# Kernel optimization log

Measured on AMD Instinct MI355X. Metric: run time of the kernel, lower is better.

The kernel has to match this reference:

```python
import jax, jax.numpy as jnp
import numpy as np

CAPACITY = 0.5  # top_k = int(seq_len * capacity)

def setup_inputs() -> dict:
    key = jax.random.key(0)
    k1, k2, k3, k4 = jax.random.split(key, 4)
    b, s, d, d_ff = 4, 4096, 1024, 4096
    x = jax.random.normal(k1, (b, s, d), dtype=jnp.float32)
    mask = jnp.ones((b, s), dtype=jnp.bool_)
    # learned params: router (Linear(d,1,bias=False)) and the block MLP
    Wr = jax.random.normal(k2, (d, 1), dtype=jnp.float32) * (d ** -0.5)
    W1 = jax.random.normal(k3, (d, d_ff), dtype=jnp.float32) * (d ** -0.5)
    W2 = jax.random.normal(k4, (d_ff, d), dtype=jnp.float32) * (d_ff ** -0.5)
    return {"x": x, "mask": mask, "Wr": Wr, "W1": W1, "W2": W2}

def reference(x, mask, Wr, W1, W2):
    b, s, d = x.shape
    top_k = int(s * CAPACITY)
    # router logits [b, s]
    logits = (x @ Wr)[..., 0]
    # top-k over sequence dim (torch sorted=False; softmax/gather are
    # permutation-equivariant so sorted top_k gives identical results)
    vals, idx = jax.lax.top_k(logits, top_k)          # [b, k]
    order = jnp.argsort(idx, axis=1)                  # sort selected indices ascending
    sel = jnp.take_along_axis(idx, order, axis=1)     # [b, k] token positions, ascending
    w = jax.nn.softmax(vals, axis=1)                  # softmax over selected logits
    r_w = jnp.take_along_axis(w, order, axis=1)       # weights reordered to match sel
    # gather selected tokens
    fx = jnp.take_along_axis(x, sel[..., None], axis=1)  # [b, k, d]
    # block: residual MLP whose update is scaled by router weights (mask unused by MLP)
    h = jax.nn.silu(fx @ W1) @ W2
    out = fx + h * r_w[..., None]
    # scatter processed tokens back into x
    batch = jnp.arange(b)[:, None]
    hidden_states = x.at[batch, sel].set(out)
    # aux loss: faithful to the original (flat view + flat index set, then BCE-with-logits mean)
    flat_logits = logits.reshape(-1)                  # [b*s]
    targets = jnp.zeros_like(flat_logits).at[sel.reshape(-1)].set(1.0)
    aux_loss = jnp.mean(
        jnp.maximum(flat_logits, 0.0)
        - flat_logits * targets
        + jnp.log1p(jnp.exp(-jnp.abs(flat_logits)))
    )
    return hidden_states, aux_loss
```

## Files before the change

kernel.cpp:

```cpp
#include <hip/hip_runtime.h>
#include <hip/hip_bf16.h>
#include <cstdint>

#define B_ 4
#define S_ 4096
#define D_ 1024
#define DFF_ 4096
#define KSEL_ 2048
#define M_ (B_ * KSEL_)
#define NTOK_ (B_ * S_)

typedef short bf16x8 __attribute__((ext_vector_type(8)));
typedef float f32x4 __attribute__((ext_vector_type(4)));

__device__ inline unsigned short f2bf(float f) {
    union { float f; unsigned int u; } c; c.f = f;
    unsigned int u = c.u;
    unsigned int r = u + 0x7fffu + ((u >> 16) & 1u);
    return (unsigned short)(r >> 16);
}

__global__ __launch_bounds__(256)
void transpose_bf16(const float* __restrict__ src, unsigned short* __restrict__ dst,
                    int R, int C) {
    __shared__ float tile[32][33];
    int c0 = blockIdx.x * 32, r0 = blockIdx.y * 32;
    for (int i = threadIdx.y; i < 32; i += 8)
        tile[i][threadIdx.x] = src[(size_t)(r0 + i) * C + c0 + threadIdx.x];
    __syncthreads();
    for (int i = threadIdx.y; i < 32; i += 8)
        dst[(size_t)(c0 + i) * R + r0 + threadIdx.x] = f2bf(tile[threadIdx.x][i]);
}

__global__ __launch_bounds__(256)
void router_kernel(const float* __restrict__ x, const float* __restrict__ Wr,
                   float* __restrict__ logits, unsigned short* __restrict__ xb,
                   float* __restrict__ out) {
    int wid = threadIdx.x >> 6, lane = threadIdx.x & 63;
    int row = blockIdx.x * 4 + wid;
    const float* xr = x + (size_t)row * D_;
    unsigned short* xbr = xb + (size_t)row * D_;
    float* outr = out + (size_t)row * D_;
    float acc = 0.f;
#pragma unroll
    for (int j = 0; j < 4; j++) {
        int off = j * 256 + lane * 4;
        float4 v = *(const float4*)(xr + off);
        float4 w = *(const float4*)(Wr + off);
        acc += v.x * w.x + v.y * w.y + v.z * w.z + v.w * w.w;
        *(float4*)(outr + off) = v;
        ushort4 o;
        o.x = f2bf(v.x); o.y = f2bf(v.y); o.z = f2bf(v.z); o.w = f2bf(v.w);
        *(ushort4*)(xbr + off) = o;
    }
#pragma unroll
    for (int s = 32; s; s >>= 1) acc += __shfl_xor(acc, s);
    if (lane == 0) logits[row] = acc;
}

__global__ __launch_bounds__(256)
void rank_partial_kernel(const float* __restrict__ logits, int* __restrict__ rank) {
    __shared__ float lj[512];
    int b  = blockIdx.x >> 7;
    int ic = (blockIdx.x >> 3) & 15;
    int jc = blockIdx.x & 7;
    const float* L = logits + b * S_;
    for (int t = threadIdx.x; t < 512; t += 256) lj[t] = L[jc * 512 + t];
    __syncthreads();
    int i = ic * 256 + threadIdx.x;
    float li = L[i];
    int jbase = jc * 512;
    int r = 0;
    const float4* __restrict__ lj4 = (const float4*)lj;
#pragma unroll 4
    for (int q = 0; q < 128; q++) {
        float4 v = lj4[q];
        int jb = jbase + q * 4;
        r += (v.x > li) | ((v.x == li) & (jb     < i));
        r += (v.y > li) | ((v.y == li) & (jb + 1 < i));
        r += (v.z > li) | ((v.z == li) & (jb + 2 < i));
        r += (v.w > li) | ((v.w == li) & (jb + 3 < i));
    }
    atomicAdd(&rank[b * S_ + i], r);
}

__global__ __launch_bounds__(256)
void compact_kernel(const float* __restrict__ logits, const int* __restrict__ rank,
                    int* __restrict__ flags,
                    int* __restrict__ rowidx, float* __restrict__ rw) {
    __shared__ float lg[S_];
    __shared__ int f[S_];
    __shared__ int tsum[256];
    __shared__ float red[256];
    int b = blockIdx.x;
    const float* L = logits + b * S_;
    const int* R = rank + b * S_;
    int* F = flags + b * S_;
    for (int j = threadIdx.x; j < S_ / 4; j += 256) {
        ((float4*)lg)[j] = ((const float4*)L)[j];
        int4 rk = ((const int4*)R)[j];
        int4 fl;
        fl.x = rk.x < KSEL_; fl.y = rk.y < KSEL_;
        fl.z = rk.z < KSEL_; fl.w = rk.w < KSEL_;
        ((int4*)f)[j] = fl;
        ((int4*)F)[j] = fl;
    }
    __syncthreads();
    float mx = -INFINITY;
    for (int j = threadIdx.x; j < S_; j += 256) mx = fmaxf(mx, lg[j]);
    red[threadIdx.x] = mx; __syncthreads();
    for (int s = 128; s; s >>= 1) {
        if (threadIdx.x < s) red[threadIdx.x] = fmaxf(red[threadIdx.x], red[threadIdx.x + s]);
        __syncthreads();
    }
    float m = red[0];
    __syncthreads();

    float esum = 0.f;
    int s0 = 0;
#pragma unroll
    for (int j = 0; j < 16; j++) {
        int i = threadIdx.x * 16 + j;
        s0 += f[i];
        if (f[i]) esum += expf(lg[i] - m);
    }
    red[threadIdx.x] = esum; __syncthreads();
    for (int s = 128; s; s >>= 1) {
        if (threadIdx.x < s) red[threadIdx.x] += red[threadIdx.x + s];
        __syncthreads();
    }
    float inv = 1.f / red[0];

    tsum[threadIdx.x] = s0; __syncthreads();
    for (int s = 1; s < 256; s <<= 1) {
        int u = (threadIdx.x >= s) ? tsum[threadIdx.x - s] : 0;
        __syncthreads();
        tsum[threadIdx.x] += u;
        __syncthreads();
    }
    int pos = tsum[threadIdx.x] - s0;
    for (int j = 0; j < 16; j++) {
        int i = threadIdx.x * 16 + j;
        if (f[i]) {
            rowidx[b * KSEL_ + pos] = b * S_ + i;
            rw[b * KSEL_ + pos] = expf(lg[i] - m) * inv;
            pos++;
        }
    }
}

__global__ __launch_bounds__(256)
void loss_kernel(const float* __restrict__ logits, const int* __restrict__ flags,
                 float* __restrict__ partials) {
    __shared__ float red[256];
    int i = blockIdx.x * 256 + threadIdx.x;
    float l = logits[i];
    float t = 0.f;
    if (i < S_)
        t = (flags[i] | flags[S_ + i] | flags[2 * S_ + i] | flags[3 * S_ + i]) ? 1.f : 0.f;
    float v = fmaxf(l, 0.f) - l * t + log1pf(expf(-fabsf(l)));
    red[threadIdx.x] = v; __syncthreads();
    for (int s = 128; s; s >>= 1) {
        if (threadIdx.x < s) red[threadIdx.x] += red[threadIdx.x + s];
        __syncthreads();
    }
    if (threadIdx.x == 0) partials[blockIdx.x] = red[0];
}

__global__ void loss_final(const float* __restrict__ partials, float* __restrict__ out) {
    float v = partials[threadIdx.x];
#pragma unroll
    for (int s = 32; s; s >>= 1) v += __shfl_xor(v, s);
    if (threadIdx.x == 0) out[0] = v / (float)NTOK_;
}

template <int MODE>
__global__ __launch_bounds__(256)
void gemm_bt_kernel(const unsigned short* __restrict__ A,
                    const unsigned short* __restrict__ BT,
                    const int* __restrict__ rowidx,
                    const float* __restrict__ rw,
                    const float* __restrict__ x,
                    unsigned short* __restrict__ Hout,
                    float* __restrict__ Out,
                    int K, int N) {
    __shared__ __attribute__((aligned(16))) unsigned short As[128 * 64];
    __shared__ __attribute__((aligned(16))) unsigned short Bs[128 * 64];
    const int tid = threadIdx.x;
    const int w = tid >> 6, lane = tid & 63;
    const int wm = w >> 1, wn = w & 1;
    const int tile_m = blockIdx.y * 128;
    const int tile_n = blockIdx.x * 128;

    const int srow = lane >> 3;
    const int sw = (lane & 7) ^ srow;
    const uint64_t abase = (uint64_t)(uintptr_t)A;
    const uint64_t bbase = (uint64_t)(uintptr_t)BT;
    uint64_t aaddr[4], baddr[4];
#pragma unroll
    for (int t = 0; t < 4; ++t) {
        int r = t * 32 + w * 8 + srow;
        int am = tile_m + r;
        int ar = (MODE == 1) ? rowidx[am] : am;
        aaddr[t] = abase + ((uint64_t)ar * K + (uint64_t)sw * 8) * 2ull;
        int bn = tile_n + r;
        baddr[t] = bbase + ((uint64_t)bn * K + (uint64_t)sw * 8) * 2ull;
    }

    f32x4 acc[4][4];
#pragma unroll
    for (int i = 0; i < 4; i++)
#pragma unroll
        for (int j = 0; j < 4; j++) acc[i][j] = (f32x4){0.f, 0.f, 0.f, 0.f};

    const int lr = lane & 15, quad = lane >> 4;
    const int KI = K >> 6;
    for (int it = 0; it < KI; ++it) {
        const uint64_t koff = (uint64_t)(it * 64) * 2ull;
#pragma unroll
        for (int t = 0; t < 4; ++t) {
            unsigned short* ldsA = &As[(t * 32 + w * 8) * 64];
            unsigned short* ldsB = &Bs[(t * 32 + w * 8) * 64];
            __builtin_amdgcn_global_load_lds(
                (const __attribute__((address_space(1))) unsigned int*)(uintptr_t)(aaddr[t] + koff),
                (__attribute__((address_space(3))) unsigned int*)ldsA, 16, 0, 0);
            __builtin_amdgcn_global_load_lds(
                (const __attribute__((address_space(1))) unsigned int*)(uintptr_t)(baddr[t] + koff),
                (__attribute__((address_space(3))) unsigned int*)ldsB, 16, 0, 0);
        }
        __syncthreads();
#pragma unroll
        for (int ks = 0; ks < 2; ++ks) {
            bf16x8 af[4], bfr[4];
#pragma unroll
            for (int t4 = 0; t4 < 4; ++t4) {
                int row = wm * 64 + t4 * 16 + lr;
                int kc = ks * 4 + quad;
                af[t4] = *(const bf16x8*)((const char*)As + row * 128 + ((kc ^ (lr & 7)) * 16));
                int nr = wn * 64 + t4 * 16 + lr;
                bfr[t4] = *(const bf16x8*)((const char*)Bs + nr * 128 + ((kc ^ (lr & 7)) * 16));
            }
#pragma unroll
            for (int ti = 0; ti < 4; ++ti)
#pragma unroll
                for (int tj = 0; tj < 4; ++tj)
                    acc[ti][tj] = __builtin_amdgcn_mfma_f32_16x16x32_bf16(
                        af[ti], bfr[tj], acc[ti][tj], 0, 0, 0);
        }
        __syncthreads();
    }

    if (MODE == 1) {
#pragma unroll
        for (int ti = 0; ti < 4; ++ti)
#pragma unroll
            for (int r = 0; r < 4; ++r) {
                int m = tile_m + wm * 64 + ti * 16 + quad * 4 + r;
#pragma unroll
                for (int tj = 0; tj < 4; ++tj) {
                    int col = tile_n + wn * 64 + tj * 16 + lr;
                    float v = acc[ti][tj][r];
                    v = v / (1.f + __expf(-v));
                    Hout[(uint64_t)m * N + col] = f2bf(v);
                }
            }
    } else {
#pragma unroll
        for (int ti = 0; ti < 4; ++ti)
#pragma unroll
            for (int r = 0; r < 4; ++r) {
                int m = tile_m + wm * 64 + ti * 16 + quad * 4 + r;
                int grow = rowidx[m];
                float wgt = rw[m];
                uint64_t rb = (uint64_t)grow * D_;
#pragma unroll
                for (int tj = 0; tj < 4; ++tj) {
                    int col = tile_n + wn * 64 + tj * 16 + lr;
                    Out[rb + col] = x[rb + col] + acc[ti][tj][r] * wgt;
                }
            }
    }
}

extern "C" void kernel_launch(void* const* d_in, const int* in_sizes, int n_in,
                              void* d_out, int out_size, void* d_ws, size_t ws_size,
                              hipStream_t stream) {
    const float* x  = (const float*)d_in[0];
    const float* Wr = (const float*)d_in[2];
    const float* W1 = (const float*)d_in[3];
    const float* W2 = (const float*)d_in[4];
    float* out = (float*)d_out;

    char* ws = (char*)d_ws;
    size_t off = 0;
    auto alloc = [&](size_t bytes) {
        char* p = ws + off;
        off = (off + bytes + 255) & ~(size_t)255;
        return p;
    };
    unsigned short* xb   = (unsigned short*)alloc((size_t)NTOK_ * D_ * 2);
    unsigned short* W1bT = (unsigned short*)alloc((size_t)DFF_ * D_ * 2);
    unsigned short* W2bT = (unsigned short*)alloc((size_t)D_ * DFF_ * 2);
    unsigned short* H    = (unsigned short*)alloc((size_t)M_ * DFF_ * 2);
    float* logits  = (float*)alloc(NTOK_ * 4);
    int*   rank    = (int*)alloc(NTOK_ * 4);
    int*   flags   = (int*)alloc(NTOK_ * 4);
    int*   rowidx  = (int*)alloc(M_ * 4);
    float* rwp     = (float*)alloc(M_ * 4);
    float* partials = (float*)alloc(64 * 4);

    (void)hipMemsetAsync(rank, 0, NTOK_ * 4, stream);

    transpose_bf16<<<dim3(DFF_ / 32, D_ / 32), dim3(32, 8), 0, stream>>>(W1, W1bT, D_, DFF_);
    transpose_bf16<<<dim3(D_ / 32, DFF_ / 32), dim3(32, 8), 0, stream>>>(W2, W2bT, DFF_, D_);
    router_kernel<<<NTOK_ / 4, 256, 0, stream>>>(x, Wr, logits, xb, out);
    rank_partial_kernel<<<512, 256, 0, stream>>>(logits, rank);
    compact_kernel<<<B_, 256, 0, stream>>>(logits, rank, flags, rowidx, rwp);
    loss_kernel<<<NTOK_ / 256, 256, 0, stream>>>(logits, flags, partials);
    loss_final<<<1, 64, 0, stream>>>(partials, out + (size_t)NTOK_ * D_);
    gemm_bt_kernel<1><<<dim3(DFF_ / 128, M_ / 128), 256, 0, stream>>>(
        xb, W1bT, rowidx, nullptr, nullptr, H, nullptr, D_, DFF_);
    gemm_bt_kernel<2><<<dim3(D_ / 128, M_ / 128), 256, 0, stream>>>(
        H, W2bT, rowidx, rwp, x, nullptr, out, DFF_, D_);
}
```

Baseline: 370.1 us.

## Pipeline GEMMs with triple-buffered LDS prefetch, larger tiles, and XCD-aware block swizzle

Replaces the single-buffered 128x128 GEMM with a 128x256 tile, 512-thread kernel that prefetches two K-steps ahead into a three-slot LDS ring and waits on vmcnt instead of issuing a full syncthreads per step. Block IDs are remapped so consecutive tiles land on the same XCD, which improves L2 reuse. MFMA sections are wrapped in s_setprio so compute waves get priority. The larger LDS footprint and 512 threads with launch bounds (512,2) can limit occupancy and raise register pressure.

```diff
diff --git a/kernel.cpp b/kernel.cpp
--- a/kernel.cpp
+++ b/kernel.cpp
@@ -174,109 +174,154 @@
     if (threadIdx.x == 0) out[0] = v / (float)NTOK_;
 }
 
-template <int MODE>
-__global__ __launch_bounds__(256)
-void gemm_bt_kernel(const unsigned short* __restrict__ A,
-                    const unsigned short* __restrict__ BT,
-                    const int* __restrict__ rowidx,
-                    const float* __restrict__ rw,
-                    const float* __restrict__ x,
-                    unsigned short* __restrict__ Hout,
-                    float* __restrict__ Out,
-                    int K, int N) {
-    __shared__ __attribute__((aligned(16))) unsigned short As[128 * 64];
-    __shared__ __attribute__((aligned(16))) unsigned short Bs[128 * 64];
+template <int MODE, int N, int K>
+__global__ __launch_bounds__(512, 2)
+void gemm_pipe_kernel(const unsigned short* __restrict__ A,
+                      const unsigned short* __restrict__ BT,
+                      const int* __restrict__ rowidx,
+                      const float* __restrict__ rw,
+                      const float* __restrict__ x,
+                      unsigned short* __restrict__ Hout,
+                      float* __restrict__ Out) {
+    constexpr int BM = 128, BN = 256, BK = 64;
+    constexpr int KI = K / BK;
+    constexpr int NT = N / BN;
+    constexpr int MT = M_ / BM;
+    constexpr int NWG = NT * MT;
+    constexpr int CPX = NWG / 8;
+    __shared__ __attribute__((aligned(16))) unsigned short As[3][BM * BK];
+    __shared__ __attribute__((aligned(16))) unsigned short Bs[3][BN * BK];
+
     const int tid = threadIdx.x;
     const int w = tid >> 6, lane = tid & 63;
-    const int wm = w >> 1, wn = w & 1;
-    const int tile_m = blockIdx.y * 128;
-    const int tile_n = blockIdx.x * 128;
+    const int wm = w >> 2, wn = w & 3;
+
+    int wgid = blockIdx.y * NT + blockIdx.x;
+    int swz = (wgid & 7) * CPX + (wgid >> 3);
+    const int tile_n = (swz % NT) * BN;
+    const int tile_m = (swz / NT) * BM;
 
     const int srow = lane >> 3;
     const int sw = (lane & 7) ^ srow;
     const uint64_t abase = (uint64_t)(uintptr_t)A;
     const uint64_t bbase = (uint64_t)(uintptr_t)BT;
-    uint64_t aaddr[4], baddr[4];
+    uint64_t aaddr[2], baddr[4];
+#pragma unroll
+    for (int t = 0; t < 2; ++t) {
+        int r = t * 64 + w * 8 + srow;
+        int ar = (MODE == 1) ? rowidx[tile_m + r] : (tile_m + r);
+        aaddr[t] = abase + ((uint64_t)ar * K + (uint64_t)sw * 8) * 2ull;
+    }
 #pragma unroll
     for (int t = 0; t < 4; ++t) {
-        int r = t * 32 + w * 8 + srow;
-        int am = tile_m + r;
-        int ar = (MODE == 1) ? rowidx[am] : am;
-        aaddr[t] = abase + ((uint64_t)ar * K + (uint64_t)sw * 8) * 2ull;
-        int bn = tile_n + r;
-        baddr[t] = bbase + ((uint64_t)bn * K + (uint64_t)sw * 8) * 2ull;
-    }
-
-    f32x4 acc[4][4];
-#pragma unroll
-    for (int i = 0; i < 4; i++)
-#pragma unroll
-        for (int j = 0; j < 4; j++) acc[i][j] = (f32x4){0.f, 0.f, 0.f, 0.f};
-
-    const int lr = lane & 15, quad = lane >> 4;
-    const int KI = K >> 6;
-    for (int it = 0; it < KI; ++it) {
-        const uint64_t koff = (uint64_t)(it * 64) * 2ull;
-#pragma unroll
-        for (int t = 0; t < 4; ++t) {
-            unsigned short* ldsA = &As[(t * 32 + w * 8) * 64];
-            unsigned short* ldsB = &Bs[(t * 32 + w * 8) * 64];
+        int r = t * 64 + w * 8 + srow;
+        baddr[t] = bbase + ((uint64_t)(tile_n + r) * K + (uint64_t)sw * 8) * 2ull;
+    }
+
+    auto stage = [&](int kt, int slot) {
+        const uint64_t koff = (uint64_t)kt * (BK * 2);
+#pragma unroll
+        for (int t = 0; t < 2; ++t) {
+            unsigned short* lds = &As[slot][(t * 64 + w * 8) * BK];
             __builtin_amdgcn_global_load_lds(
                 (const __attribute__((address_space(1))) unsigned int*)(uintptr_t)(aaddr[t] + koff),
-                (__attribute__((address_space(3))) unsigned int*)ldsA, 16, 0, 0);
+                (__attribute__((address_space(3))) unsigned int*)lds, 16, 0, 0);
+        }
+#pragma unroll
+        for (int t = 0; t < 4; ++t) {
+            unsigned short* lds = &Bs[slot][(t * 64 + w * 8) * BK];
             __builtin_amdgcn_global_load_lds(
                 (const __attribute__((address_space(1))) unsigned int*)(uintptr_t)(baddr[t] + koff),
-                (__attribute__((address_space(3))) unsigned int*)ldsB, 16, 0, 0);
-        }
-        __syncthreads();
-#pragma unroll
-        for (int ks = 0; ks < 2; ++ks) {
-            bf16x8 af[4], bfr[4];
-#pragma unroll
-            for (int t4 = 0; t4 < 4; ++t4) {
-                int row = wm * 64 + t4 * 16 + lr;
+                (__attribute__((address_space(3))) unsigned int*)lds, 16, 0, 0);
+        }
+    };
+
+    f32x4 acc[4][4];
+#pragma unroll
+    for (int i = 0; i < 4; i++)
+#pragma unroll
+        for (int j = 0; j < 4; j++) acc[i][j] = (f32x4){0.f, 0.f, 0.f, 0.f};
+
+    stage(0, 0);
+    stage(1, 1);
+    asm volatile("s_waitcnt vmcnt(6)" ::: "memory");
+    __builtin_amdgcn_s_barrier();
+
+    const int lr = lane & 15, quad = lane >> 4;
+    int s_cur = 0;
+    for (int kt = 0; kt < KI; ++kt) {
+        int s_pre = s_cur + 2; if (s_pre >= 3) s_pre -= 3;
+        if (kt + 2 < KI) stage(kt + 2, s_pre);
+
+        bf16x8 af[4][2], bfr[4][2];
+#pragma unroll
+        for (int m4 = 0; m4 < 4; ++m4) {
+            int row = wm * 64 + m4 * 16 + lr;
+#pragma unroll
+            for (int ks = 0; ks < 2; ++ks) {
                 int kc = ks * 4 + quad;
-                af[t4] = *(const bf16x8*)((const char*)As + row * 128 + ((kc ^ (lr & 7)) * 16));
-                int nr = wn * 64 + t4 * 16 + lr;
-                bfr[t4] = *(const bf16x8*)((const char*)Bs + nr * 128 + ((kc ^ (lr & 7)) * 16));
+                af[m4][ks] = *(const bf16x8*)((const char*)&As[s_cur][0]
+                                + row * (BK * 2) + ((kc ^ (lr & 7)) * 16));
             }
-#pragma unroll
-            for (int ti = 0; ti < 4; ++ti)
-#pragma unroll
-                for (int tj = 0; tj < 4; ++tj)
-                    acc[ti][tj] = __builtin_amdgcn_mfma_f32_16x16x32_bf16(
-                        af[ti], bfr[tj], acc[ti][tj], 0, 0, 0);
-        }
-        __syncthreads();
+        }
+#pragma unroll
+        for (int n4 = 0; n4 < 4; ++n4) {
+            int col = wn * 64 + n4 * 16 + lr;
+#pragma unroll
+            for (int ks = 0; ks < 2; ++ks) {
+                int kc = ks * 4 + quad;
+                bfr[n4][ks] = *(const bf16x8*)((const char*)&Bs[s_cur][0]
+                                + col * (BK * 2) + ((kc ^ (lr & 7)) * 16));
+            }
+        }
+
+        __builtin_amdgcn_s_setprio(1);
+#pragma unroll
+        for (int ks = 0; ks < 2; ++ks)
+#pragma unroll
+            for (int m4 = 0; m4 < 4; ++m4)
+#pragma unroll
+                for (int n4 = 0; n4 < 4; ++n4)
+                    acc[m4][n4] = __builtin_amdgcn_mfma_f32_16x16x32_bf16(
+                        af[m4][ks], bfr[n4][ks], acc[m4][n4], 0, 0, 0);
+        __builtin_amdgcn_s_setprio(0);
+
+        if (kt + 2 < KI) {
+            asm volatile("s_waitcnt vmcnt(6)" ::: "memory");
+        } else {
+            asm volatile("s_waitcnt vmcnt(0)" ::: "memory");
+        }
+        __builtin_amdgcn_s_barrier();
+        s_cur += 1; if (s_cur >= 3) s_cur = 0;
     }
 
     if (MODE == 1) {
 #pragma unroll
-        for (int ti = 0; ti < 4; ++ti)
+        for (int m4 = 0; m4 < 4; ++m4)
 #pragma unroll
             for (int r = 0; r < 4; ++r) {
-                int m = tile_m + wm * 64 + ti * 16 + quad * 4 + r;
-#pragma unroll
-                for (int tj = 0; tj < 4; ++tj) {
-                    int col = tile_n + wn * 64 + tj * 16 + lr;
-                    float v = acc[ti][tj][r];
+                int m = tile_m + wm * 64 + m4 * 16 + quad * 4 + r;
+#pragma unroll
+                for (int n4 = 0; n4 < 4; ++n4) {
+                    int col = tile_n + wn * 64 + n4 * 16 + lr;
+                    float v = acc[m4][n4][r];
                     v = v / (1.f + __expf(-v));
                     Hout[(uint64_t)m * N + col] = f2bf(v);
                 }
             }
     } else {
 #pragma unroll
-        for (int ti = 0; ti < 4; ++ti)
+        for (int m4 = 0; m4 < 4; ++m4)
 #pragma unroll
             for (int r = 0; r < 4; ++r) {
-                int m = tile_m + wm * 64 + ti * 16 + quad * 4 + r;
+                int m = tile_m + wm * 64 + m4 * 16 + quad * 4 + r;
                 int grow = rowidx[m];
                 float wgt = rw[m];
                 uint64_t rb = (uint64_t)grow * D_;
 #pragma unroll
-                for (int tj = 0; tj < 4; ++tj) {
-                    int col = tile_n + wn * 64 + tj * 16 + lr;
-                    Out[rb + col] = x[rb + col] + acc[ti][tj][r] * wgt;
+                for (int n4 = 0; n4 < 4; ++n4) {
+                    int col = tile_n + wn * 64 + n4 * 16 + lr;
+                    Out[rb + col] = x[rb + col] + acc[m4][n4][r] * wgt;
                 }
             }
     }
@@ -318,8 +363,8 @@
     compact_kernel<<<B_, 256, 0, stream>>>(logits, rank, flags, rowidx, rwp);
     loss_kernel<<<NTOK_ / 256, 256, 0, stream>>>(logits, flags, partials);
     loss_final<<<1, 64, 0, stream>>>(partials, out + (size_t)NTOK_ * D_);
-    gemm_bt_kernel<1><<<dim3(DFF_ / 128, M_ / 128), 256, 0, stream>>>(
-        xb, W1bT, rowidx, nullptr, nullptr, H, nullptr, D_, DFF_);
-    gemm_bt_kernel<2><<<dim3(D_ / 128, M_ / 128), 256, 0, stream>>>(
-        H, W2bT, rowidx, rwp, x, nullptr, out, DFF_, D_);
-}
+    gemm_pipe_kernel<1, DFF_, D_><<<dim3(DFF_ / 256, M_ / 128), 512, 0, stream>>>(
+        xb, W1bT, rowidx, nullptr, nullptr, H, nullptr);
+    gemm_pipe_kernel<2, D_, DFF_><<<dim3(D_ / 256, M_ / 128), 512, 0, stream>>>(
+        H, W2bT, rowidx, rwp, x, nullptr, out);
+}
```

After: 395.9 us. +7.0%, slower.
